# Kernel tuning notes

Hardware: AMD Instinct MI355X
Metric: run time of the kernel (lower is better)

## Reference

```python
import jax, jax.numpy as jnp
import numpy as np

B, S, D = 2, 2048, 1024
H = 16
HD = D // H
E = 8          # num_experts
TOPK = 2
DF = 4 * D     # expert hidden
LN_EPS = 1e-5


def _layer_norm(h, g, b):
    mu = jnp.mean(h, axis=-1, keepdims=True)
    var = jnp.mean(jnp.square(h - mu), axis=-1, keepdims=True)
    return (h - mu) * jax.lax.rsqrt(var + LN_EPS) * g + b


def setup_inputs() -> dict:
    key = jax.random.key(0)
    ks = jax.random.split(key, 12)
    s = lambda fan: 1.0 / np.sqrt(fan)
    return {
        "x": jax.random.normal(ks[0], (B, S, D), jnp.float32),
        "ln1_g": jnp.ones((D,), jnp.float32),
        "ln1_b": jnp.zeros((D,), jnp.float32),
        "ln2_g": jnp.ones((D,), jnp.float32),
        "ln2_b": jnp.zeros((D,), jnp.float32),
        "wqkv": jax.random.normal(ks[1], (D, 3 * D), jnp.float32) * s(D),
        "bqkv": jnp.zeros((3 * D,), jnp.float32),
        "wo": jax.random.normal(ks[2], (D, D), jnp.float32) * s(D),
        "bo": jnp.zeros((D,), jnp.float32),
        "w_router": jax.random.normal(ks[3], (D, E), jnp.float32) * s(D),
        "w1": jax.random.normal(ks[4], (E, D, DF), jnp.float32) * s(D),
        "b1": jnp.zeros((E, DF), jnp.float32),
        "w2": jax.random.normal(ks[5], (E, DF, D), jnp.float32) * s(DF),
        "b2": jnp.zeros((E, D), jnp.float32),
    }


def reference(x, ln1_g, ln1_b, ln2_g, ln2_b, wqkv, bqkv, wo, bo,
              w_router, w1, b1, w2, b2):
    # ---- pre-norm causal self-attention (dropout = identity in eval) ----
    h = _layer_norm(x, ln1_g, ln1_b)
    qkv = h @ wqkv + bqkv                                  # [B,S,3D]
    qkv = qkv.reshape(B, S, 3, H, HD)
    q, k, v = (jnp.moveaxis(qkv[:, :, i], 1, 2) for i in range(3))  # [B,H,S,HD]
    scores = jnp.einsum("bhqd,bhkd->bhqk", q, k) / np.sqrt(HD)
    causal = jnp.tril(jnp.ones((S, S), bool))
    scores = jnp.where(causal, scores, jnp.finfo(scores.dtype).min)
    attn = jax.nn.softmax(scores, axis=-1)
    ctx = jnp.einsum("bhqk,bhkd->bhqd", attn, v)           # [B,H,S,HD]
    ctx = jnp.moveaxis(ctx, 1, 2).reshape(B, S, D)
    x = x + (ctx @ wo + bo)

    # ---- pre-norm top-2 MoE FFN ----
    h2 = _layer_norm(x, ln2_g, ln2_b)
    t = h2.reshape(B * S, D)                               # tokens [T,D]
    logits = t @ w_router                                  # [T,E]
    probs = jax.nn.softmax(logits, axis=-1)
    top_v, top_i = jax.lax.top_k(probs, TOPK)              # [T,2]
    top_v = top_v / jnp.sum(top_v, axis=-1, keepdims=True)
    # combine gates as dense [T,E] (zero for unselected experts)
    gates = jnp.sum(jax.nn.one_hot(top_i, E, dtype=t.dtype) * top_v[..., None], axis=1)
    # dense all-expert compute, weighted combine (same math as sparse dispatch)
    hid = jax.nn.gelu(jnp.einsum("td,edf->etf", t, w1) + b1[:, None, :], approximate=False)
    eout = jnp.einsum("etf,efd->etd", hid, w2) + b2[:, None, :]   # [E,T,D]
    ffn_out = jnp.einsum("etd,te->td", eout, gates).reshape(B, S, D)

    return x + ffn_out
```

## Files before the change

### kernel.cpp

```cpp
#include <hip/hip_runtime.h>
#include <hip/hip_bf16.h>
#include <math.h>

#define NB    2
#define SEQ   2048
#define DMODEL 1024
#define NH    16
#define HDIM  64
#define NE    8
#define DFF   4096
#define TTOK  4096

#define MT_MAX   72
#define SLOT_MAX 9216

#define C_CNT  0
#define C_FILL 8
#define C_BASE 16
#define C_NMT  24
#define C_MTE  32
#define C_MTS  104

typedef __attribute__((ext_vector_type(8))) short short8;
typedef __attribute__((ext_vector_type(4))) float f32x4;
typedef __attribute__((ext_vector_type(4))) unsigned int uint4v;

static __device__ __forceinline__ float bf2f(unsigned short u) {
  union { unsigned int i; float f; } c; c.i = ((unsigned int)u) << 16; return c.f;
}
static __device__ __forceinline__ unsigned short f2bf(float f) {
  unsigned int x = __float_as_uint(f);
  unsigned int r = (x + 0x7FFFu + ((x >> 16) & 1u)) >> 16;
  return (unsigned short)r;
}

static __device__ __forceinline__ void gl_lds16(const void* g, void* l) {
  __builtin_amdgcn_global_load_lds(
      (const __attribute__((address_space(1))) unsigned int*)(uintptr_t)g,
      (__attribute__((address_space(3))) unsigned int*)(uintptr_t)l,
      16, 0, 0);
}

template<int MODE>
__global__ __launch_bounds__(256) void ln_kernel(
    const float* __restrict__ x,
    const float* __restrict__ gam,
    const float* __restrict__ bet,
    float* __restrict__ outf,
    unsigned short* __restrict__ outb,
    unsigned short* __restrict__ outlo)
{
  int t = blockIdx.x, tid = threadIdx.x;
  f32x4 v = ((const f32x4*)(x + (size_t)t * DMODEL))[tid];
  float s  = v[0] + v[1] + v[2] + v[3];
  float sq = v[0]*v[0] + v[1]*v[1] + v[2]*v[2] + v[3]*v[3];
  #pragma unroll
  for (int off = 1; off < 64; off <<= 1) {
    s  += __shfl_xor(s, off);
    sq += __shfl_xor(sq, off);
  }
  __shared__ float red[8];
  int w = tid >> 6, l = tid & 63;
  if (l == 0) { red[w] = s; red[4 + w] = sq; }
  __syncthreads();
  s  = red[0] + red[1] + red[2] + red[3];
  sq = red[4] + red[5] + red[6] + red[7];
  float mu  = s * (1.0f / DMODEL);
  float var = sq * (1.0f / DMODEL) - mu * mu;
  float rs  = rsqrtf(var + 1e-5f);
  f32x4 g = ((const f32x4*)gam)[tid];
  f32x4 b = ((const f32x4*)bet)[tid];
  float r[4];
  r[0] = (v[0] - mu) * rs * g[0] + b[0];
  r[1] = (v[1] - mu) * rs * g[1] + b[1];
  r[2] = (v[2] - mu) * rs * g[2] + b[2];
  r[3] = (v[3] - mu) * rs * g[3] + b[3];
  if constexpr (MODE == 0) {
    f32x4 o = {r[0], r[1], r[2], r[3]};
    ((f32x4*)(outf + (size_t)t * DMODEL))[tid] = o;
  } else if constexpr (MODE == 1) {
    ushort4 o; o.x = f2bf(r[0]); o.y = f2bf(r[1]); o.z = f2bf(r[2]); o.w = f2bf(r[3]);
    ((ushort4*)(outb + (size_t)t * DMODEL))[tid] = o;
  } else {
    ushort4 hi, lo;
    unsigned short h0 = f2bf(r[0]); hi.x = h0; lo.x = f2bf(r[0] - bf2f(h0));
    unsigned short h1 = f2bf(r[1]); hi.y = h1; lo.y = f2bf(r[1] - bf2f(h1));
    unsigned short h2 = f2bf(r[2]); hi.z = h2; lo.z = f2bf(r[2] - bf2f(h2));
    unsigned short h3 = f2bf(r[3]); hi.w = h3; lo.w = f2bf(r[3] - bf2f(h3));
    ((ushort4*)(outb  + (size_t)t * DMODEL))[tid] = hi;
    ((ushort4*)(outlo + (size_t)t * DMODEL))[tid] = lo;
  }
}

template<int EPI>
__global__ __launch_bounds__(256) void mgemm_split(
    const unsigned short* __restrict__ Ah,
    const unsigned short* __restrict__ Alo,
    const unsigned short* __restrict__ Bth,
    const unsigned short* __restrict__ Btl,
    const float* __restrict__ bias,
    const float* __restrict__ resid,
    float* __restrict__ C, int M, int N, int K)
{
  __shared__ unsigned short AH[128][32];
  __shared__ unsigned short AL[128][32];
  __shared__ unsigned short BH[128][32];
  __shared__ unsigned short BL[128][32];
  int tid = threadIdx.x;
  int l = tid & 63, wv = tid >> 6;
  int wr = wv >> 1, wc = wv & 1;
  int m0 = blockIdx.y * 128, n0 = blockIdx.x * 128;
  int rsub = l >> 2, csub = (l & 3) * 8;
  int row0 = wv * 32 + rsub, row1 = row0 + 16;

  const unsigned short* gah0 = Ah  + (size_t)(m0 + row0) * K + csub;
  const unsigned short* gah1 = Ah  + (size_t)(m0 + row1) * K + csub;
  const unsigned short* gal0 = Alo + (size_t)(m0 + row0) * K + csub;
  const unsigned short* gal1 = Alo + (size_t)(m0 + row1) * K + csub;
  const unsigned short* gbh0 = Bth + (size_t)(n0 + row0) * K + csub;
  const unsigned short* gbh1 = Bth + (size_t)(n0 + row1) * K + csub;
  const unsigned short* gbl0 = Btl + (size_t)(n0 + row0) * K + csub;
  const unsigned short* gbl1 = Btl + (size_t)(n0 + row1) * K + csub;

  const f32x4 z = {0.f, 0.f, 0.f, 0.f};
  f32x4 acc[4][4];
  #pragma unroll
  for (int i = 0; i < 4; ++i)
    #pragma unroll
    for (int j = 0; j < 4; ++j) acc[i][j] = z;

  for (int k0 = 0; k0 < K; k0 += 32) {
    __syncthreads();
    gl_lds16(gah0 + k0, &AH[wv * 32][0]);
    gl_lds16(gah1 + k0, &AH[wv * 32 + 16][0]);
    gl_lds16(gal0 + k0, &AL[wv * 32][0]);
    gl_lds16(gal1 + k0, &AL[wv * 32 + 16][0]);
    gl_lds16(gbh0 + k0, &BH[wv * 32][0]);
    gl_lds16(gbh1 + k0, &BH[wv * 32 + 16][0]);
    gl_lds16(gbl0 + k0, &BL[wv * 32][0]);
    gl_lds16(gbl1 + k0, &BL[wv * 32 + 16][0]);
    __syncthreads();

    short8 afh[4], afl[4], bfh[4], bfl[4];
    #pragma unroll
    for (int m = 0; m < 4; ++m) {
      afh[m] = *(const short8*)(&AH[wr * 64 + m * 16 + (l & 15)][(l >> 4) << 3]);
      afl[m] = *(const short8*)(&AL[wr * 64 + m * 16 + (l & 15)][(l >> 4) << 3]);
    }
    #pragma unroll
    for (int n = 0; n < 4; ++n) {
      bfh[n] = *(const short8*)(&BH[wc * 64 + n * 16 + (l & 15)][(l >> 4) << 3]);
      bfl[n] = *(const short8*)(&BL[wc * 64 + n * 16 + (l & 15)][(l >> 4) << 3]);
    }
    #pragma unroll
    for (int m = 0; m < 4; ++m)
      #pragma unroll
      for (int n = 0; n < 4; ++n) {
        acc[m][n] = __builtin_amdgcn_mfma_f32_16x16x32_bf16(afh[m], bfh[n], acc[m][n], 0, 0, 0);
        acc[m][n] = __builtin_amdgcn_mfma_f32_16x16x32_bf16(afl[m], bfh[n], acc[m][n], 0, 0, 0);
        acc[m][n] = __builtin_amdgcn_mfma_f32_16x16x32_bf16(afh[m], bfl[n], acc[m][n], 0, 0, 0);
      }
  }

  int rbase = m0 + wr * 64 + ((l >> 4) << 2);
  int cbase = n0 + wc * 64 + (l & 15);
  #pragma unroll
  for (int n = 0; n < 4; ++n) {
    int col = cbase + n * 16;
    float bv = bias[col];
    #pragma unroll
    for (int m = 0; m < 4; ++m) {
      #pragma unroll
      for (int r = 0; r < 4; ++r) {
        int row = rbase + m * 16 + r;
        float v = acc[m][n][r] + bv;
        if constexpr (EPI == 1) v += resid[(size_t)row * N + col];
        C[(size_t)row * N + col] = v;
      }
    }
  }
}

__global__ __launch_bounds__(256) void qkv_split(
    const float* __restrict__ qkv,
    unsigned short* __restrict__ Qh, unsigned short* __restrict__ Ql,
    unsigned short* __restrict__ Kh, unsigned short* __restrict__ Kl,
    unsigned short* __restrict__ Vth, unsigned short* __restrict__ Vtl)
{
  __shared__ float Vt[64][68];
  int st = blockIdx.x, bh = blockIdx.y;
  int b = bh >> 4, h = bh & 15;
  int tid = threadIdx.x;
  int row = tid >> 2, cs = (tid & 3) * 16;
  size_t hb = (size_t)bh * SEQ * 64;
  int srow = st * 64 + row;
  size_t src = (size_t)(b * SEQ + srow) * 3072 + (size_t)h * HDIM + cs;

  #pragma unroll
  for (int qk = 0; qk < 2; ++qk) {
    const float* p = qkv + src + qk * 1024;
    unsigned short hi8[16], lo8[16];
    #pragma unroll
    for (int i = 0; i < 16; ++i) {
      float v = p[i];
      unsigned short hh_ = f2bf(v);
      hi8[i] = hh_; lo8[i] = f2bf(v - bf2f(hh_));
    }
    unsigned short* dh = (qk ? Kh : Qh) + hb + (size_t)srow * 64 + cs;
    unsigned short* dl = (qk ? Kl : Ql) + hb + (size_t)srow * 64 + cs;
    *(uint4v*)dh       = *(const uint4v*)&hi8[0];
    *(uint4v*)(dh + 8) = *(const uint4v*)&hi8[8];
    *(uint4v*)dl       = *(const uint4v*)&lo8[0];
    *(uint4v*)(dl + 8) = *(const uint4v*)&lo8[8];
  }
  {
    const float* p = qkv + src + 2048;
    #pragma unroll
    for (int i = 0; i < 4; ++i)
      *(f32x4*)&Vt[row][cs + i * 4] = *(const f32x4*)(p + i * 4);
  }
  __syncthreads();
  {
    int d = tid >> 2, ks = (tid & 3) * 16;
    unsigned short hi8[16], lo8[16];
    #pragma unroll
    for (int j = 0; j < 16; ++j) {
      float v = Vt[ks + j][d];
      unsigned short hh_ = f2bf(v);
      hi8[j] = hh_; lo8[j] = f2bf(v - bf2f(hh_));
    }
    size_t dst = hb + (size_t)d * SEQ + st * 64 + ks;
    *(uint4v*)(Vth + dst)     = *(const uint4v*)&hi8[0];
    *(uint4v*)(Vth + dst + 8) = *(const uint4v*)&hi8[8];
    *(uint4v*)(Vtl + dst)     = *(const uint4v*)&lo8[0];
    *(uint4v*)(Vtl + dst + 8) = *(const uint4v*)&lo8[8];
  }
}

__global__ __launch_bounds__(256) void attn_mf3(
    const unsigned short* __restrict__ Qh, const unsigned short* __restrict__ Ql,
    const unsigned short* __restrict__ Kh, const unsigned short* __restrict__ Kl,
    const unsigned short* __restrict__ Vth, const unsigned short* __restrict__ Vtl,
    float* __restrict__ paro,
    float* __restrict__ parml)
{
  __shared__ unsigned short KVh[64][72], KVl[64][72];
  __shared__ unsigned short Phs[64][72], Pls[64][72];
  int bh = blockIdx.y;
  int b = bh >> 4, h = bh & 15;
  int bx = blockIdx.x;
  int p  = bx >> 1, par = bx & 1;
  int tid = threadIdx.x, wv = tid >> 6, l = tid & 63;
  int lm = l & 15, lh = l >> 4;
  const size_t hb = (size_t)bh * SEQ * 64;
  int srow = tid >> 2, scs = (tid & 3) * 16;
  int qin = wv * 16 + lh * 4;
  const f32x4 z = {0.f, 0.f, 0.f, 0.f};

  #pragma unroll 1
  for (int job = 0; job < 2; ++job) {
    int qt = job ? (31 - p) : p;
    int q0 = qt * 64 + wv * 16;

    short8 aQh[2], aQl[2];
    {
      size_t qa = hb + (size_t)(q0 + lm) * 64 + (lh << 3);
      aQh[0] = *(const short8*)(Qh + qa);
      aQh[1] = *(const short8*)(Qh + qa + 32);
      aQl[0] = *(const short8*)(Ql + qa);
      aQl[1] = *(const short8*)(Ql + qa + 32);
    }
    f32x4 ctx[4] = {z, z, z, z};
    float mrun[4] = {-1e4f, -1e4f, -1e4f, -1e4f};
    float lrun[4] = {0.f, 0.f, 0.f, 0.f};

    for (int kt = par; kt <= qt; kt += 2) {
      uint4v vh0, vh1, vl0, vl1;
      {
        size_t vg = hb + (size_t)srow * SEQ + kt * 64 + scs;
        vh0 = *(const uint4v*)(Vth + vg);
        vh1 = *(const uint4v*)(Vth + vg + 8);
        vl0 = *(const uint4v*)(Vtl + vg);
        vl1 = *(const uint4v*)(Vtl + vg + 8);
      }
      __syncthreads();
      {
        size_t kg = hb + (size_t)(kt * 64 + srow) * 64 + scs;
        *(uint4v*)&KVh[srow][scs]     = *(const uint4v*)(Kh + kg);
        *(uint4v*)&KVh[srow][scs + 8] = *(const uint4v*)(Kh + kg + 8);
        *(uint4v*)&KVl[srow][scs]     = *(const uint4v*)(Kl + kg);
        *(uint4v*)&KVl[srow][scs + 8] = *(const uint4v*)(Kl + kg + 8);
      }
      __syncthreads();

      f32x4 S4[4] = {z, z, z, z};
      #pragma unroll
      for (int n = 0; n < 4; ++n) {
        #pragma unroll
        for (int c = 0; c < 2; ++c) {
          short8 kbh = *(const short8*)&KVh[n * 16 + lm][c * 32 + (lh << 3)];
          short8 kbl = *(const short8*)&KVl[n * 16 + lm][c * 32 + (lh << 3)];
          S4[n] = __builtin_amdgcn_mfma_f32_16x16x32_bf16(aQh[c], kbh, S4[n], 0, 0, 0);
          S4[n] = __builtin_amdgcn_mfma_f32_16x16x32_bf16(aQl[c], kbh, S4[n], 0, 0, 0);
          S4[n] = __builtin_amdgcn_mfma_f32_16x16x32_bf16(aQh[c], kbl, S4[n], 0, 0, 0);
        }
      }
      bool diag = (kt == qt);
      #pragma unroll
      for (int r = 0; r < 4; ++r) {
        float s0 = S4[0][r] * 0.125f, s1 = S4[1][r] * 0.125f;
        float s2 = S4[2][r] * 0.125f, s3 = S4[3][r] * 0.125f;
        if (diag) {
          int qq = qin + r;
          if (lm      > qq) s0 = -1e30f;
          if (16 + lm > qq) s1 = -1e30f;
          if (32 + lm > qq) s2 = -1e30f;
          if (48 + lm > qq) s3 = -1e30f;
        }
        float cm = fmaxf(fmaxf(s0, s1), fmaxf(s2, s3));
        cm = fmaxf(cm, __shfl_xor(cm, 1));
        cm = fmaxf(cm, __shfl_xor(cm, 2));
        cm = fmaxf(cm, __shfl_xor(cm, 4));
        cm = fmaxf(cm, __shfl_xor(cm, 8));
        if (cm > mrun[r] + 8.0f) {
          float sc = __expf(mrun[r] - cm);
          lrun[r] *= sc;
          ctx[0][r] *= sc; ctx[1][r] *= sc; ctx[2][r] *= sc; ctx[3][r] *= sc;
          mrun[r] = cm;
        }
        float p0 = __expf(s0 - mrun[r]), p1 = __expf(s1 - mrun[r]);
        float p2 = __expf(s2 - mrun[r]), p3 = __expf(s3 - mrun[r]);
        float rs = (p0 + p1) + (p2 + p3);
        rs += __shfl_xor(rs, 1); rs += __shfl_xor(rs, 2);
        rs += __shfl_xor(rs, 4); rs += __shfl_xor(rs, 8);
        lrun[r] += rs;
        int prow = qin + r;
        unsigned short e0 = f2bf(p0); Phs[prow][lm]      = e0; Pls[prow][lm]      = f2bf(p0 - bf2f(e0));
        unsigned short e1 = f2bf(p1); Phs[prow][16 + lm] = e1; Pls[prow][16 + lm] = f2bf(p1 - bf2f(e1));
        unsigned short e2 = f2bf(p2); Phs[prow][32 + lm] = e2; Pls[prow][32 + lm] = f2bf(p2 - bf2f(e2));
        unsigned short e3 = f2bf(p3); Phs[prow][48 + lm] = e3; Pls[prow][48 + lm] = f2bf(p3 - bf2f(e3));
      }
      __syncthreads();
      {
        *(uint4v*)&KVh[srow][scs]     = vh0;
        *(uint4v*)&KVh[srow][scs + 8] = vh1;
        *(uint4v*)&KVl[srow][scs]     = vl0;
        *(uint4v*)&KVl[srow][scs + 8] = vl1;
      }
      __syncthreads();

      #pragma unroll
      for (int c = 0; c < 2; ++c) {
        short8 pah = *(const short8*)&Phs[wv * 16 + lm][c * 32 + (lh << 3)];
        short8 pal = *(const short8*)&Pls[wv * 16 + lm][c * 32 + (lh << 3)];
        #pragma unroll
        for (int n = 0; n < 4; ++n) {
          short8 vbh = *(const short8*)&KVh[n * 16 + lm][c * 32 + (lh << 3)];
          short8 vbl = *(const short8*)&KVl[n * 16 + lm][c * 32 + (lh << 3)];
          ctx[n] = __builtin_amdgcn_mfma_f32_16x16x32_bf16(pah, vbh, ctx[n], 0, 0, 0);
          ctx[n] = __builtin_amdgcn_mfma_f32_16x16x32_bf16(pal, vbh, ctx[n], 0, 0, 0);
          ctx[n] = __builtin_amdgcn_mfma_f32_16x16x32_bf16(pah, vbl, ctx[n], 0, 0, 0);
        }
      }
    }

    #pragma unroll
    for (int r = 0; r < 4; ++r) {
      int qg = b * SEQ + qt * 64 + wv * 16 + lh * 4 + r;
      size_t ob = ((size_t)par * TTOK + qg) * DMODEL + (size_t)h * HDIM + lm;
      #pragma unroll
      for (int n = 0; n < 4; ++n) paro[ob + n * 16] = ctx[n][r];
      if (lm == 0) {
        size_t mb = (((size_t)par * TTOK + qg) * NH + h) * 2;
        parml[mb] = mrun[r]; parml[mb + 1] = lrun[r];
      }
    }
  }
}

template<int NS>
__global__ __launch_bounds__(256) void attn_merge(
    const float* __restrict__ paro,
    const float* __restrict__ parml,
    unsigned short* __restrict__ ctxh,
    unsigned short* __restrict__ ctxl)
{
  int gid = blockIdx.x * 256 + threadIdx.x;
  int ds = gid & 3;
  int h  = (gid >> 2) & 15;
  int t  = gid >> 6;
  float m[NS], lv[NS];
  float mx = -1e30f;
  #pragma unroll
  for (int i = 0; i < NS; ++i) {
    size_t mb = (((size_t)i * TTOK + t) * NH + h) * 2;
    m[i] = parml[mb]; lv[i] = parml[mb + 1];
    mx = fmaxf(mx, m[i]);
  }
  float w[NS], lsum = 0.f;
  #pragma unroll
  for (int i = 0; i < NS; ++i) { w[i] = __expf(m[i] - mx); lsum += lv[i] * w[i]; }
  float inv = 1.0f / lsum;
  size_t ob = (size_t)t * DMODEL + (size_t)h * HDIM + ds * 16;
  #pragma unroll
  for (int i4 = 0; i4 < 4; ++i4) {
    f32x4 v = {0.f, 0.f, 0.f, 0.f};
    #pragma unroll
    for (int i = 0; i < NS; ++i) {
      const f32x4* oi = (const f32x4*)(paro + (size_t)i * TTOK * DMODEL + ob);
      v += oi[i4] * w[i];
    }
    v = v * inv;
    ushort4 hi, lo;
    unsigned short e0 = f2bf(v[0]); hi.x = e0; lo.x = f2bf(v[0] - bf2f(e0));
    unsigned short e1 = f2bf(v[1]); hi.y = e1; lo.y = f2bf(v[1] - bf2f(e1));
    unsigned short e2 = f2bf(v[2]); hi.z = e2; lo.z = f2bf(v[2] - bf2f(e2));
    unsigned short e3 = f2bf(v[3]); hi.w = e3; lo.w = f2bf(v[3] - bf2f(e3));
    *(ushort4*)(ctxh + ob + i4 * 4) = hi;
    *(ushort4*)(ctxl + ob + i4 * 4) = lo;
  }
}

__global__ __launch_bounds__(256) void router_kernel(
    const float* __restrict__ x1,
    const float* __restrict__ gam,
    const float* __restrict__ bet,
    const float* __restrict__ wrt,
    int* __restrict__ ctrl,
    int2* __restrict__ t_e,
    float2* __restrict__ t_g)
{
  int w = threadIdx.x >> 6, l = threadIdx.x & 63;
  int t = blockIdx.x * 4 + w;
  const f32x4* row = (const f32x4*)(x1 + (size_t)t * DMODEL);
  f32x4 v[4];
  float s = 0.f, sq = 0.f;
  #pragma unroll
  for (int i = 0; i < 4; ++i) {
    v[i] = row[l + i * 64];
    #pragma unroll
    for (int j = 0; j < 4; ++j) { s += v[i][j]; sq += v[i][j] * v[i][j]; }
  }
  #pragma unroll
  for (int off = 1; off < 64; off <<= 1) {
    s  += __shfl_xor(s, off);
    sq += __shfl_xor(sq, off);
  }
  float mu  = s * (1.0f / DMODEL);
  float var = sq * (1.0f / DMODEL) - mu * mu;
  float rs  = rsqrtf(var + 1e-5f);

  float acc[NE] = {0.f, 0.f, 0.f, 0.f, 0.f, 0.f, 0.f, 0.f};
  #pragma unroll
  for (int i = 0; i < 4; ++i) {
    int base = (l + i * 64) * 4;
    #pragma unroll
    for (int j = 0; j < 4; ++j) {
      int idx = base + j;
      float xn = (v[i][j] - mu) * rs * gam[idx] + bet[idx];
      const f32x4* wr0 = (const f32x4*)(wrt + idx * NE);
      f32x4 w0 = wr0[0], w1v = wr0[1];
      acc[0] += xn * w0[0]; acc[1] += xn * w0[1];
      acc[2] += xn * w0[2]; acc[3] += xn * w0[3];
      acc[4] += xn * w1v[0]; acc[5] += xn * w1v[1];
      acc[6] += xn * w1v[2]; acc[7] += xn * w1v[3];
    }
  }
  #pragma unroll
  for (int e = 0; e < NE; ++e) {
    #pragma unroll
    for (int off = 1; off < 64; off <<= 1) acc[e] += __shfl_xor(acc[e], off);
  }
  if (l == 0) {
    int e0 = 0; float m0v = acc[0];
    #pragma unroll
    for (int e = 1; e < NE; ++e) if (acc[e] > m0v) { m0v = acc[e]; e0 = e; }
    int e1 = -1; float m1v = -1e30f;
    #pragma unroll
    for (int e = 0; e < NE; ++e) if (e != e0 && acc[e] > m1v) { m1v = acc[e]; e1 = e; }
    float r = __expf(m1v - m0v);
    float g0 = 1.0f / (1.0f + r);
    float g1 = r * g0;
    t_e[t] = make_int2(e0, e1);
    t_g[t] = make_float2(g0, g1);
    atomicAdd(&ctrl[C_CNT + e0], 1);
    atomicAdd(&ctrl[C_CNT + e1], 1);
  }
}

__global__ void scan_kernel(int* __restrict__ ctrl)
{
  if (threadIdx.x == 0 && blockIdx.x == 0) {
    int b = 0, m = 0;
    for (int e = 0; e < NE; ++e) {
      ctrl[C_BASE + e] = b;
      int pc = (ctrl[C_CNT + e] + 127) & ~127;
      int nt = pc >> 7;
      for (int i = 0; i < nt; ++i) {
        ctrl[C_MTE + m] = e;
        ctrl[C_MTS + m] = b + (i << 7);
        ++m;
      }
      b += pc;
    }
    ctrl[C_NMT] = m;
  }
}

__global__ __launch_bounds__(256) void gather_kernel(
    int* __restrict__ ctrl,
    const int2* __restrict__ t_e,
    const float2* __restrict__ t_g,
    int* __restrict__ slot_token,
    float* __restrict__ slot_gate)
{
  int t = blockIdx.x * 256 + threadIdx.x;
  int2 e = t_e[t];
  float2 g = t_g[t];
  int p0 = atomicAdd(&ctrl[C_FILL + e.x], 1);
  int s0 = ctrl[C_BASE + e.x] + p0;
  slot_token[s0] = t; slot_gate[s0] = g.x;
  int p1 = atomicAdd(&ctrl[C_FILL + e.y], 1);
  int s1 = ctrl[C_BASE + e.y] + p1;
  slot_token[s1] = t; slot_gate[s1] = g.y;
}

__global__ __launch_bounds__(256) void transpose_conv(
    const float* __restrict__ in, unsigned short* __restrict__ outb,
    unsigned short* __restrict__ outlo, int K, int N)
{
  __shared__ float T[64][68];
  int e = blockIdx.z;
  int n0 = blockIdx.x * 64, k0 = blockIdx.y * 64;
  const float* src = in + (size_t)e * K * N;
  unsigned short* dst = outb + (size_t)e * K * N;
  unsigned short* dstl = outlo ? outlo + (size_t)e * K * N : nullptr;
  int tid = threadIdx.x;
  int r = tid >> 4, c4 = (tid & 15) * 4;
  #pragma unroll
  for (int i = 0; i < 4; ++i) {
    f32x4 v = *(const f32x4*)(src + (size_t)(k0 + r + i * 16) * N + n0 + c4);
    *(f32x4*)(&T[r + i * 16][c4]) = v;
  }
  __syncthreads();
  #pragma unroll
  for (int i = 0; i < 4; ++i) {
    int rr = r + i * 16;
    float v0 = T[c4 + 0][rr], v1 = T[c4 + 1][rr];
    float v2 = T[c4 + 2][rr], v3 = T[c4 + 3][rr];
    ushort4 o;
    o.x = f2bf(v0); o.y = f2bf(v1); o.z = f2bf(v2); o.w = f2bf(v3);
    *(ushort4*)(dst + (size_t)(n0 + rr) * K + k0 + c4) = o;
    if (dstl) {
      ushort4 lo;
      lo.x = f2bf(v0 - bf2f(o.x));
      lo.y = f2bf(v1 - bf2f(o.y));
      lo.z = f2bf(v2 - bf2f(o.z));
      lo.w = f2bf(v3 - bf2f(o.w));
      *(ushort4*)(dstl + (size_t)(n0 + rr) * K + k0 + c4) = lo;
    }
  }
}

__global__ __launch_bounds__(256) void moe_w1f(
    const unsigned short* __restrict__ h2,
    const unsigned short* __restrict__ w1t,
    const float* __restrict__ b1,
    const int* __restrict__ ctrl,
    const int* __restrict__ slot_token,
    unsigned short* __restrict__ Hs)
{
  int mt = blockIdx.y;
  if (mt >= ctrl[C_NMT]) return;
  int e = ctrl[C_MTE + mt];
  int slot0 = ctrl[C_MTS + mt];
  const int N = DFF, K = DMODEL;
  const unsigned short* Bt = w1t + (size_t)e * K * N;
  const float* bias = b1 + (size_t)e * DFF;

  __shared__ unsigned short Al[128][32];
  __shared__ unsigned short Bl[128][32];
  __shared__ int tokrow[128];
  int tid = threadIdx.x;
  if (tid < 128) {
    int tk = slot_token[slot0 + tid];
    tokrow[tid] = tk < 0 ? 0 : tk;
  }
  __syncthreads();
  int l = tid & 63, wv = tid >> 6;
  int wr = wv >> 1, wc = wv & 1;
  int n0 = blockIdx.x * 128;
  int rsub = l >> 2, csub = (l & 3) * 8;
  int row0 = wv * 32 + rsub, row1 = row0 + 16;
  const unsigned short* ga0 = h2 + (size_t)tokrow[row0] * DMODEL + csub;
  const unsigned short* ga1 = h2 + (size_t)tokrow[row1] * DMODEL + csub;
  const unsigned short* gb0 = Bt + (size_t)(n0 + row0) * K + csub;
  const unsigned short* gb1 = Bt + (size_t)(n0 + row1) * K + csub;

  const f32x4 z = {0.f, 0.f, 0.f, 0.f};
  f32x4 acc[4][4];
  #pragma unroll
  for (int i = 0; i < 4; ++i)
    #pragma unroll
    for (int j = 0; j < 4; ++j) acc[i][j] = z;

  for (int k0 = 0; k0 < K; k0 += 32) {
    __syncthreads();
    gl_lds16(ga0 + k0, &Al[wv * 32][0]);
    gl_lds16(ga1 + k0, &Al[wv * 32 + 16][0]);
    gl_lds16(gb0 + k0, &Bl[wv * 32][0]);
    gl_lds16(gb1 + k0, &Bl[wv * 32 + 16][0]);
    __syncthreads();

    short8 af[4], bfr[4];
    #pragma unroll
    for (int m = 0; m < 4; ++m)
      af[m] = *(const short8*)(&Al[wr * 64 + m * 16 + (l & 15)][(l >> 4) << 3]);
    #pragma unroll
    for (int n = 0; n < 4; ++n)
      bfr[n] = *(const short8*)(&Bl[wc * 64 + n * 16 + (l & 15)][(l >> 4) << 3]);
    #pragma unroll
    for (int m = 0; m < 4; ++m)
      #pragma unroll
      for (int n = 0; n < 4; ++n)
        acc[m][n] = __builtin_amdgcn_mfma_f32_16x16x32_bf16(af[m], bfr[n], acc[m][n], 0, 0, 0);
  }

  int rbase = wr * 64 + ((l >> 4) << 2);
  int cbase = n0 + wc * 64 + (l & 15);
  #pragma unroll
  for (int n = 0; n < 4; ++n) {
    int col = cbase + n * 16;
    float bv = bias[col];
    #pragma unroll
    for (int m = 0; m < 4; ++m) {
      #pragma unroll
      for (int r = 0; r < 4; ++r) {
        int srow = slot0 + rbase + m * 16 + r;
        float v = acc[m][n][r] + bv;
        v = 0.5f * v * (1.0f + erff(v * 0.70710678118654752f));
        Hs[(size_t)srow * DFF + col] = f2bf(v);
      }
    }
  }
}

__global__ __launch_bounds__(256) void moe_w2f(
    const unsigned short* __restrict__ Hs,
    const unsigned short* __restrict__ w2t,
    const float* __restrict__ b2,
    const int* __restrict__ ctrl,
    const int* __restrict__ slot_token,
    const float* __restrict__ slot_gate,
    float* __restrict__ ffn)
{
  int mt = blockIdx.y;
  if (mt >= ctrl[C_NMT]) return;
  int e = ctrl[C_MTE + mt];
  int slot0 = ctrl[C_MTS + mt];
  const int N = DMODEL, K = DFF;
  const unsigned short* Bt = w2t + (size_t)e * (size_t)K * N;
  const float* bias = b2 + (size_t)e * DMODEL;

  __shared__ unsigned short Al[128][32];
  __shared__ unsigned short Bl[128][32];
  int tid = threadIdx.x;
  int l = tid & 63, wv = tid >> 6;
  int wr = wv >> 1, wc = wv & 1;
  int n0 = blockIdx.x * 128;
  int rsub = l >> 2, csub = (l & 3) * 8;
  int row0 = wv * 32 + rsub, row1 = row0 + 16;
  const unsigned short* ga0 = Hs + (size_t)(slot0 + row0) * DFF + csub;
  const unsigned short* ga1 = Hs + (size_t)(slot0 + row1) * DFF + csub;
  const unsigned short* gb0 = Bt + (size_t)(n0 + row0) * K + csub;
  const unsigned short* gb1 = Bt + (size_t)(n0 + row1) * K + csub;

  const f32x4 z = {0.f, 0.f, 0.f, 0.f};
  f32x4 acc[4][4];
  #pragma unroll
  for (int i = 0; i < 4; ++i)
    #pragma unroll
    for (int j = 0; j < 4; ++j) acc[i][j] = z;

  for (int k0 = 0; k0 < K; k0 += 32) {
    __syncthreads();
    gl_lds16(ga0 + k0, &Al[wv * 32][0]);
    gl_lds16(ga1 + k0, &Al[wv * 32 + 16][0]);
    gl_lds16(gb0 + k0, &Bl[wv * 32][0]);
    gl_lds16(gb1 + k0, &Bl[wv * 32 + 16][0]);
    __syncthreads();

    short8 af[4], bfr[4];
    #pragma unroll
    for (int m = 0; m < 4; ++m)
      af[m] = *(const short8*)(&Al[wr * 64 + m * 16 + (l & 15)][(l >> 4) << 3]);
    #pragma unroll
    for (int n = 0; n < 4; ++n)
      bfr[n] = *(const short8*)(&Bl[wc * 64 + n * 16 + (l & 15)][(l >> 4) << 3]);
    #pragma unroll
    for (int m = 0; m < 4; ++m)
      #pragma unroll
      for (int n = 0; n < 4; ++n)
        acc[m][n] = __builtin_amdgcn_mfma_f32_16x16x32_bf16(af[m], bfr[n], acc[m][n], 0, 0, 0);
  }

  int rbase = wr * 64 + ((l >> 4) << 2);
  int cbase = n0 + wc * 64 + (l & 15);
  #pragma unroll
  for (int n = 0; n < 4; ++n) {
    int col = cbase + n * 16;
    float bv = bias[col];
    #pragma unroll
    for (int m = 0; m < 4; ++m) {
      #pragma unroll
      for (int r = 0; r < 4; ++r) {
        int srow = slot0 + rbase + m * 16 + r;
        int tok = slot_token[srow];
        if (tok >= 0) {
          float v = acc[m][n][r] + bv;
          atomicAdd(&ffn[(size_t)tok * DMODEL + col], slot_gate[srow] * v);
        }
      }
    }
  }
}

__global__ __launch_bounds__(256) void final_add(
    const float* __restrict__ x1,
    const float* __restrict__ ffn,
    float* __restrict__ out)
{
  int i = blockIdx.x * 256 + threadIdx.x;
  f32x4 xr = ((const f32x4*)x1)[i];
  f32x4 fr = ((const f32x4*)ffn)[i];
  f32x4 o;
  o[0] = xr[0] + fr[0];
  o[1] = xr[1] + fr[1];
  o[2] = xr[2] + fr[2];
  o[3] = xr[3] + fr[3];
  ((f32x4*)out)[i] = o;
}

extern "C" void kernel_launch(void* const* d_in, const int* in_sizes, int n_in,
                              void* d_out, int out_size, void* d_ws, size_t ws_size,
                              hipStream_t stream) {
  (void)in_sizes; (void)n_in; (void)out_size;
  const float* x     = (const float*)d_in[0];
  const float* ln1_g = (const float*)d_in[1];
  const float* ln1_b = (const float*)d_in[2];
  const float* ln2_g = (const float*)d_in[3];
  const float* ln2_b = (const float*)d_in[4];
  const float* wqkv  = (const float*)d_in[5];
  const float* bqkv  = (const float*)d_in[6];
  const float* wo    = (const float*)d_in[7];
  const float* bo    = (const float*)d_in[8];
  const float* wrt   = (const float*)d_in[9];
  const float* w1    = (const float*)d_in[10];
  const float* b1    = (const float*)d_in[11];
  const float* w2    = (const float*)d_in[12];
  const float* b2    = (const float*)d_in[13];
  float* out = (float*)d_out;

  char* ws = (char*)d_ws;
  size_t off = 0;
  auto alloc = [&](size_t bytes) -> void* {
    void* p = ws + off;
    off += (bytes + 255) & ~(size_t)255;
    return p;
  };
  float*          x1    = (float*)alloc((size_t)TTOK * DMODEL * 4);
  unsigned short* h2    = (unsigned short*)alloc((size_t)TTOK * DMODEL * 2);
  int*            ctrl  = (int*)alloc(1024);
  int2*           t_e   = (int2*)alloc((size_t)TTOK * 8);
  float2*         t_g   = (float2*)alloc((size_t)TTOK * 8);
  int*            slot_token = (int*)alloc((size_t)SLOT_MAX * 4);
  float*          slot_gate  = (float*)alloc((size_t)SLOT_MAX * 4);
  float*          P1    = (float*)alloc((size_t)TTOK * DMODEL * 4);
  char*           P2    = (char*)alloc((size_t)SLOT_MAX * DFF * 2);
  unsigned short* w1t   = (unsigned short*)alloc((size_t)NE * DMODEL * DFF * 2);
  unsigned short* w2t   = (unsigned short*)alloc((size_t)NE * DFF * DMODEL * 2);
  unsigned short* wqkvTh = (unsigned short*)alloc((size_t)DMODEL * 3 * DMODEL * 2);
  unsigned short* wqkvTl = (unsigned short*)alloc((size_t)DMODEL * 3 * DMODEL * 2);
  unsigned short* woTh  = (unsigned short*)alloc((size_t)DMODEL * DMODEL * 2);
  unsigned short* woTl  = (unsigned short*)alloc((size_t)DMODEL * DMODEL * 2);
  unsigned short* hh    = (unsigned short*)alloc((size_t)TTOK * DMODEL * 2);
  unsigned short* hl    = (unsigned short*)alloc((size_t)TTOK * DMODEL * 2);
  unsigned short* ctxh  = (unsigned short*)alloc((size_t)TTOK * DMODEL * 2);
  unsigned short* ctxl  = (unsigned short*)alloc((size_t)TTOK * DMODEL * 2);
  size_t headsz = (size_t)NB * NH * SEQ * HDIM;
  unsigned short* Qh  = (unsigned short*)alloc(headsz * 2);
  unsigned short* Ql  = (unsigned short*)alloc(headsz * 2);
  unsigned short* Khp = (unsigned short*)alloc(headsz * 2);
  unsigned short* Klp = (unsigned short*)alloc(headsz * 2);
  unsigned short* Vth = (unsigned short*)alloc(headsz * 2);
  unsigned short* Vtl = (unsigned short*)alloc(headsz * 2);
  float*          paro2  = (float*)alloc((size_t)2 * TTOK * DMODEL * 4);
  float*          parml2 = (float*)alloc((size_t)2 * TTOK * NH * 2 * 4);

  float*          qkv  = (float*)P2;
  float*          ffn  = P1;
  unsigned short* Hs   = (unsigned short*)P2;

  hipMemsetAsync(ctrl, 0, 16 * 4, stream);
  hipMemsetAsync(slot_token, 0xFF, (size_t)SLOT_MAX * 4, stream);

  transpose_conv<<<dim3(DFF / 64, DMODEL / 64, NE), 256, 0, stream>>>(
      w1, w1t, nullptr, DMODEL, DFF);
  transpose_conv<<<dim3(DMODEL / 64, DFF / 64, NE), 256, 0, stream>>>(
      w2, w2t, nullptr, DFF, DMODEL);
  transpose_conv<<<dim3(3 * DMODEL / 64, DMODEL / 64, 1), 256, 0, stream>>>(
      wqkv, wqkvTh, wqkvTl, DMODEL, 3 * DMODEL);
  transpose_conv<<<dim3(DMODEL / 64, DMODEL / 64, 1), 256, 0, stream>>>(
      wo, woTh, woTl, DMODEL, DMODEL);

  ln_kernel<2><<<TTOK, 256, 0, stream>>>(x, ln1_g, ln1_b, nullptr, hh, hl);
  mgemm_split<0><<<dim3(3 * DMODEL / 128, TTOK / 128), 256, 0, stream>>>(
      hh, hl, wqkvTh, wqkvTl, bqkv, nullptr, qkv, TTOK, 3 * DMODEL, DMODEL);
  qkv_split<<<dim3(SEQ / 64, NB * NH), 256, 0, stream>>>(
      qkv, Qh, Ql, Khp, Klp, Vth, Vtl);
  attn_mf3<<<dim3(32, NB * NH), 256, 0, stream>>>(
      Qh, Ql, Khp, Klp, Vth, Vtl, paro2, parml2);
  attn_merge<2><<<(TTOK * NH * 4) / 256, 256, 0, stream>>>(
      paro2, parml2, ctxh, ctxl);
  mgemm_split<1><<<dim3(DMODEL / 128, TTOK / 128), 256, 0, stream>>>(
      ctxh, ctxl, woTh, woTl, bo, x, x1, TTOK, DMODEL, DMODEL);

  ln_kernel<1><<<TTOK, 256, 0, stream>>>(x1, ln2_g, ln2_b, nullptr, h2, nullptr);
  router_kernel<<<TTOK / 4, 256, 0, stream>>>(x1, ln2_g, ln2_b, wrt, ctrl, t_e, t_g);
  scan_kernel<<<1, 64, 0, stream>>>(ctrl);
  gather_kernel<<<TTOK / 256, 256, 0, stream>>>(ctrl, t_e, t_g, slot_token, slot_gate);
  hipMemsetAsync(ffn, 0, (size_t)TTOK * DMODEL * 4, stream);
  moe_w1f<<<dim3(DFF / 128, MT_MAX), 256, 0, stream>>>(
      h2, w1t, b1, ctrl, slot_token, Hs);
  moe_w2f<<<dim3(DMODEL / 128, MT_MAX), 256, 0, stream>>>(
      Hs, w2t, b2, ctrl, slot_token, slot_gate, ffn);
  final_add<<<(TTOK * DMODEL / 4) / 256, 256, 0, stream>>>(x1, ffn, out);
}
```

Measured before the change: 902.3 us.

## Double-buffer LDS tiles in MoE W2 GEMM to overlap loads with MFMA

Converts the moe_w2f kernel's K-loop from a load-sync-compute pattern to a two-stage LDS ping-pong. The next K-slice's global-to-LDS loads are issued before computing on the current slice, with an explicit vmcnt wait and barriers replacing the two __syncthreads per iteration. The aim is to hide global memory latency behind the MFMA work. It doubles LDS use and relies on hand-placed waitcnt and barriers, so it is sensitive to compiler scheduling.

Result: no change. 892.9 us (-1.0%).

```diff
diff --git a/kernel.cpp b/kernel.cpp
--- a/kernel.cpp
+++ b/kernel.cpp
@@ -662,8 +662,8 @@
   const unsigned short* Bt = w2t + (size_t)e * (size_t)K * N;
   const float* bias = b2 + (size_t)e * DMODEL;
 
-  __shared__ unsigned short Al[128][32];
-  __shared__ unsigned short Bl[128][32];
+  __shared__ unsigned short Al[2][128][32];
+  __shared__ unsigned short Bl[2][128][32];
   int tid = threadIdx.x;
   int l = tid & 63, wv = tid >> 6;
   int wr = wv >> 1, wc = wv & 1;
@@ -682,26 +682,38 @@
     #pragma unroll
     for (int j = 0; j < 4; ++j) acc[i][j] = z;
 
-  for (int k0 = 0; k0 < K; k0 += 32) {
-    __syncthreads();
-    gl_lds16(ga0 + k0, &Al[wv * 32][0]);
-    gl_lds16(ga1 + k0, &Al[wv * 32 + 16][0]);
-    gl_lds16(gb0 + k0, &Bl[wv * 32][0]);
-    gl_lds16(gb1 + k0, &Bl[wv * 32 + 16][0]);
-    __syncthreads();
+  gl_lds16(ga0, &Al[0][wv * 32][0]);
+  gl_lds16(ga1, &Al[0][wv * 32 + 16][0]);
+  gl_lds16(gb0, &Bl[0][wv * 32][0]);
+  gl_lds16(gb1, &Bl[0][wv * 32 + 16][0]);
+
+  const int nst = K / 32;
+  #pragma unroll 1
+  for (int s = 0; s < nst; ++s) {
+    int cur = s & 1, nxt = cur ^ 1;
+    int k0n = (s + 1 < nst ? s + 1 : s) * 32;
+    gl_lds16(ga0 + k0n, &Al[nxt][wv * 32][0]);
+    gl_lds16(ga1 + k0n, &Al[nxt][wv * 32 + 16][0]);
+    gl_lds16(gb0 + k0n, &Bl[nxt][wv * 32][0]);
+    gl_lds16(gb1 + k0n, &Bl[nxt][wv * 32 + 16][0]);
+    asm volatile("s_waitcnt vmcnt(4)" ::: "memory");
+    __builtin_amdgcn_sched_barrier(0);
+    __builtin_amdgcn_s_barrier();
 
     short8 af[4], bfr[4];
     #pragma unroll
     for (int m = 0; m < 4; ++m)
-      af[m] = *(const short8*)(&Al[wr * 64 + m * 16 + (l & 15)][(l >> 4) << 3]);
+      af[m] = *(const short8*)(&Al[cur][wr * 64 + m * 16 + (l & 15)][(l >> 4) << 3]);
     #pragma unroll
     for (int n = 0; n < 4; ++n)
-      bfr[n] = *(const short8*)(&Bl[wc * 64 + n * 16 + (l & 15)][(l >> 4) << 3]);
+      bfr[n] = *(const short8*)(&Bl[cur][wc * 64 + n * 16 + (l & 15)][(l >> 4) << 3]);
     #pragma unroll
     for (int m = 0; m < 4; ++m)
       #pragma unroll
       for (int n = 0; n < 4; ++n)
         acc[m][n] = __builtin_amdgcn_mfma_f32_16x16x32_bf16(af[m], bfr[n], acc[m][n], 0, 0, 0);
+
+    __builtin_amdgcn_s_barrier();
   }
 
   int rbase = wr * 64 + ((l >> 4) << 2);
```
